# Performance work log

Measured on AMD Instinct MI355X. Metric: run time of the kernel, lower is better.

The kernel has to match this reference:

```python
import jax, jax.numpy as jnp
import numpy as np
import math

L, B, S, D, DK = 12, 2, 2048, 1024, 256
LN_EPS = 1e-5


def setup_inputs() -> dict:
    key = jax.random.key(0)
    k0, k1, k2 = jax.random.split(key, 3)
    states = jax.random.normal(k0, (L, B, S, D), dtype=jnp.float32)
    # nn.Linear default init ~ U(-1/sqrt(fan_in), 1/sqrt(fan_in))
    bound = 1.0 / math.sqrt(D)
    Wq = jax.random.uniform(k1, (DK, D), minval=-bound, maxval=bound, dtype=jnp.float32)
    Wk = jax.random.uniform(k2, (DK, D), minval=-bound, maxval=bound, dtype=jnp.float32)
    ln_weight = jnp.ones((D,), dtype=jnp.float32)
    ln_bias = jnp.zeros((D,), dtype=jnp.float32)
    latest_gate = jnp.asarray(0.5, dtype=jnp.float32)
    return {"states": states, "Wq": Wq, "Wk": Wk,
            "ln_weight": ln_weight, "ln_bias": ln_bias,
            "latest_gate": latest_gate}


def _layer_norm(x, w, b):
    mu = jnp.mean(x, axis=-1, keepdims=True)
    var = jnp.mean(jnp.square(x - mu), axis=-1, keepdims=True)
    return (x - mu) * jax.lax.rsqrt(var + LN_EPS) * w + b


def reference(states, Wq, Wk, ln_weight, ln_bias, latest_gate):
    # states: (L, B, S, D)
    normalized = _layer_norm(states, ln_weight, ln_bias)          # (L,B,S,D)
    latest = normalized[-1]                                       # (B,S,D)
    query = jnp.einsum('bsd,kd->bsk', latest, Wq)                 # (B,S,DK)
    keys = jnp.einsum('lbsd,kd->lbsk', normalized, Wk)            # (L,B,S,DK)
    scale = 1.0 / math.sqrt(query.shape[-1])
    logits = jnp.einsum('bsk,lbsk->lbs', query, keys) * scale     # (L,B,S)
    weights = jax.nn.softmax(logits, axis=0)                      # softmax over depth
    mixed = jnp.einsum('lbs,lbsd->bsd', weights, states)          # (B,S,D)
    gate = jax.nn.sigmoid(latest_gate)
    return gate * states[-1] + (1.0 - gate) * mixed
```

## Files before the change

### kernel.cpp

```cpp
#include <hip/hip_runtime.h>

#define NL 12
#define NB 2
#define NS 2048
#define ND 1024
#define NDK 256
#define NBS (NB*NS)

typedef __attribute__((ext_vector_type(8))) short short8;
typedef __attribute__((ext_vector_type(4))) short short4v;
typedef __attribute__((ext_vector_type(4))) float floatx4;

__device__ __forceinline__ unsigned short f2bf(float f) {
    unsigned int u = __float_as_uint(f);
    u += 0x7FFFu + ((u >> 16) & 1u);
    return (unsigned short)(u >> 16);
}
__device__ __forceinline__ short f2bfs(float f) { return (short)f2bf(f); }
__device__ __forceinline__ float bf2f(short s) {
    return __uint_as_float(((unsigned int)(unsigned short)s) << 16);
}

__global__ void k_prep_ln(const float* __restrict__ Wq, const float* __restrict__ Wk,
                          const float* __restrict__ x11,
                          const float* __restrict__ lnw, const float* __restrict__ lnb,
                          unsigned short* __restrict__ W2t, unsigned short* __restrict__ U) {
    const int tid = threadIdx.x;
    if (blockIdx.x < 256) {
        const int lane = tid & 63, wv = tid >> 6;
        const int wid = blockIdx.x * 4 + wv;
        const int tm = wid >> 4;
        const int tnb = wid & 15;
        const int lr = lane & 15, kh = lane >> 4;
        floatx4 acc[4];
#pragma unroll
        for (int c = 0; c < 4; ++c) acc[c] = (floatx4){0.f, 0.f, 0.f, 0.f};
#pragma unroll 2
        for (int kb = 0; kb < 8; ++kb) {
            const float* Ab = Wk + (size_t)(kb * 32 + kh * 8) * ND + tm * 16 + lr;
            const float* Bb = Wq + (size_t)(kb * 32 + kh * 8) * ND + tnb * 64 + lr;
            short8 a;
#pragma unroll
            for (int j = 0; j < 8; ++j) a[j] = f2bfs(Ab[(size_t)j * ND]);
#pragma unroll
            for (int c = 0; c < 4; ++c) {
                short8 b;
#pragma unroll
                for (int j = 0; j < 8; ++j) b[j] = f2bfs(Bb[(size_t)j * ND + c * 16]);
                acc[c] = __builtin_amdgcn_mfma_f32_16x16x32_bf16(a, b, acc[c], 0, 0, 0);
            }
        }
#pragma unroll
        for (int c = 0; c < 4; ++c)
#pragma unroll
            for (int r = 0; r < 4; ++r)
                W2t[(size_t)(tm * 16 + kh * 4 + r) * ND + tnb * 64 + c * 16 + lr] = f2bf(acc[c][r]);
        return;
    }
    __shared__ float red[8];
    const int p = blockIdx.x - 256;
    const float4* xr = (const float4*)(x11 + (size_t)p * ND);
    float4 x = xr[tid];
    float s1 = x.x + x.y + x.z + x.w;
    float s2 = x.x*x.x + x.y*x.y + x.z*x.z + x.w*x.w;
#pragma unroll
    for (int m = 32; m > 0; m >>= 1) { s1 += __shfl_xor(s1, m); s2 += __shfl_xor(s2, m); }
    int wv = tid >> 6;
    if ((tid & 63) == 0) { red[wv] = s1; red[4 + wv] = s2; }
    __syncthreads();
    float S1 = red[0] + red[1] + red[2] + red[3];
    float S2 = red[4] + red[5] + red[6] + red[7];
    float mu = S1 * (1.0f / ND);
    float var = S2 * (1.0f / ND) - mu * mu;
    float rstd = rsqrtf(var + 1e-5f);
    float4 w = ((const float4*)lnw)[tid];
    float4 b = ((const float4*)lnb)[tid];
    ushort4 u;
    u.x = f2bf((x.x - mu) * rstd * w.x + b.x);
    u.y = f2bf((x.y - mu) * rstd * w.y + b.y);
    u.z = f2bf((x.z - mu) * rstd * w.z + b.z);
    u.w = f2bf((x.w - mu) * rstd * w.w + b.w);
    ((ushort4*)U)[(size_t)p * (ND / 4) + tid] = u;
}

#define BM 64
#define BN 128
#define BK 64
#define LDP 72
#define TLP 132
__global__ __launch_bounds__(256) void k_vgemm(const unsigned short* __restrict__ U,
                                               const unsigned short* __restrict__ W2t,
                                               unsigned short* __restrict__ V) {
    __shared__ unsigned short As[2][BM * LDP];
    __shared__ unsigned short Bs[2][BN * LDP];
    const int tid = threadIdx.x;
    const int lane = tid & 63;
    const int wv = tid >> 6;
    const int wr = wv >> 1, wc = wv & 1;
    const int lr = lane & 15, kh = lane >> 4;
    const int bm0 = (blockIdx.x >> 3) * BM;
    const int bn0 = (blockIdx.x & 7) * BN;

    int aOff[2], bOff[4];
    const short8* gA[2];
    const short8* gB[4];
#pragma unroll
    for (int j = 0; j < 2; ++j) {
        int idx = j * 256 + tid;
        int row = idx >> 3, c8 = idx & 7;
        aOff[j] = row * LDP + c8 * 8;
        gA[j] = (const short8*)(U + (size_t)(bm0 + row) * ND) + c8;
    }
#pragma unroll
    for (int j = 0; j < 4; ++j) {
        int idx = j * 256 + tid;
        int row = idx >> 3, c8 = idx & 7;
        bOff[j] = row * LDP + c8 * 8;
        gB[j] = (const short8*)(W2t + (size_t)(bn0 + row) * ND) + c8;
    }

    floatx4 acc[2][4];
#pragma unroll
    for (int m = 0; m < 2; ++m)
#pragma unroll
        for (int n = 0; n < 4; ++n) acc[m][n] = (floatx4){0.f, 0.f, 0.f, 0.f};

    short8 ra[2], rb[4];
#pragma unroll
    for (int j = 0; j < 2; ++j) ra[j] = gA[j][0];
#pragma unroll
    for (int j = 0; j < 4; ++j) rb[j] = gB[j][0];

    const int NT = ND / BK;
#pragma unroll 1
    for (int t = 0; t < NT; ++t) {
        unsigned short* Ab = As[t & 1];
        unsigned short* Bb = Bs[t & 1];
#pragma unroll
        for (int j = 0; j < 2; ++j) *(short8*)&Ab[aOff[j]] = ra[j];
#pragma unroll
        for (int j = 0; j < 4; ++j) *(short8*)&Bb[bOff[j]] = rb[j];
        __syncthreads();
        if (t < NT - 1) {
#pragma unroll
            for (int j = 0; j < 2; ++j) ra[j] = gA[j][(t + 1) * 8];
#pragma unroll
            for (int j = 0; j < 4; ++j) rb[j] = gB[j][(t + 1) * 8];
        }
#pragma unroll
        for (int kk = 0; kk < 2; ++kk) {
            short8 a[2], b[4];
#pragma unroll
            for (int m = 0; m < 2; ++m)
                a[m] = *(const short8*)&Ab[(wr * 32 + m * 16 + lr) * LDP + kk * 32 + kh * 8];
#pragma unroll
            for (int n = 0; n < 4; ++n)
                b[n] = *(const short8*)&Bb[(wc * 64 + n * 16 + lr) * LDP + kk * 32 + kh * 8];
#pragma unroll
            for (int m = 0; m < 2; ++m)
#pragma unroll
                for (int n = 0; n < 4; ++n)
                    acc[m][n] = __builtin_amdgcn_mfma_f32_16x16x32_bf16(a[m], b[n], acc[m][n], 0, 0, 0);
        }
    }

    __syncthreads();
    unsigned short* Cs = (unsigned short*)As;
#pragma unroll
    for (int m = 0; m < 2; ++m)
#pragma unroll
        for (int n = 0; n < 4; ++n)
#pragma unroll
            for (int r = 0; r < 4; ++r)
                Cs[(wr * 32 + m * 16 + kh * 4 + r) * TLP + wc * 64 + n * 16 + lr] = f2bf(acc[m][n][r]);
    __syncthreads();
#pragma unroll
    for (int j = 0; j < 4; ++j) {
        int idx = j * 256 + tid;
        int row = idx >> 4, c8 = idx & 15;
        *(short8*)&V[(size_t)(bm0 + row) * ND + bn0 + c8 * 8] = *(const short8*)&Cs[row * TLP + c8 * 8];
    }
}

__global__ void k_fused(const float* __restrict__ states, const unsigned short* __restrict__ V,
                        const float* __restrict__ lnw, const float* __restrict__ lnb,
                        const float* __restrict__ gatep, float* __restrict__ out) {
    __shared__ float s_logit[12];
    __shared__ float s_w12[12];
    __shared__ float s_g;
    __shared__ float s_part[4][ND];
    __shared__ float s_x11[ND];
    const int p = blockIdx.x;
    const int tid = threadIdx.x;
    const int lane = tid & 63;
    const int wv = tid >> 6;
    const size_t LS = (size_t)NBS * ND;
    const float* base = states + (size_t)p * ND;
    const short4v* Vp = (const short4v*)(V + (size_t)p * ND);

    float4 t[4];
    float red[11];
#pragma unroll
    for (int j = 0; j < 11; ++j) red[j] = 0.f;
#pragma unroll
    for (int i = 0; i < 4; ++i) {
        int idx = lane + 64 * i;
        short4v vq = Vp[idx];
        float4 v;
        v.x = bf2f(vq[0]); v.y = bf2f(vq[1]); v.z = bf2f(vq[2]); v.w = bf2f(vq[3]);
        float4 w = ((const float4*)lnw)[idx];
        float4 b = ((const float4*)lnb)[idx];
        float4 tt; tt.x = v.x*w.x; tt.y = v.y*w.y; tt.z = v.z*w.z; tt.w = v.w*w.w;
        t[i] = tt;
        red[9]  += tt.x + tt.y + tt.z + tt.w;
        red[10] += v.x*b.x + v.y*b.y + v.z*b.z + v.w*b.w;
    }

    float4 x[3][4];
#pragma unroll
    for (int rr = 0; rr < 3; ++rr) {
        const int l = wv + 4 * rr;
        const float4* xr = (const float4*)(base + (size_t)l * LS);
#pragma unroll
        for (int i = 0; i < 4; ++i) {
            float4 xx = xr[lane + 64 * i];
            x[rr][i] = xx;
            red[rr]     += xx.x + xx.y + xx.z + xx.w;
            red[3 + rr] += xx.x*xx.x + xx.y*xx.y + xx.z*xx.z + xx.w*xx.w;
            red[6 + rr] += xx.x*t[i].x + xx.y*t[i].y + xx.z*t[i].z + xx.w*t[i].w;
        }
    }
#pragma unroll
    for (int m = 32; m > 0; m >>= 1) {
#pragma unroll
        for (int j = 0; j < 11; ++j) red[j] += __shfl_xor(red[j], m);
    }
    if (lane == 0) {
#pragma unroll
        for (int rr = 0; rr < 3; ++rr) {
            float mu = red[rr] * (1.0f / ND);
            float var = red[3 + rr] * (1.0f / ND) - mu * mu;
            float rstd = rsqrtf(var + 1e-5f);
            s_logit[wv + 4 * rr] = 0.0625f * (rstd * (red[6 + rr] - mu * red[9]) + red[10]);
        }
    }
    __syncthreads();
    if (tid == 0) {
        float mx = s_logit[0];
#pragma unroll
        for (int l = 1; l < 12; ++l) mx = fmaxf(mx, s_logit[l]);
        float e[12], sum = 0.f;
#pragma unroll
        for (int l = 0; l < 12; ++l) { e[l] = expf(s_logit[l] - mx); sum += e[l]; }
        float inv = 1.0f / sum;
#pragma unroll
        for (int l = 0; l < 12; ++l) s_w12[l] = e[l] * inv;
        s_g = 1.0f / (1.0f + expf(-gatep[0]));
    }
    __syncthreads();

    const float w0 = s_w12[wv], w1 = s_w12[wv + 4], w2 = s_w12[wv + 8];
#pragma unroll
    for (int i = 0; i < 4; ++i) {
        int idx = lane + 64 * i;
        float4 pm;
        pm.x = w0*x[0][i].x + w1*x[1][i].x + w2*x[2][i].x;
        pm.y = w0*x[0][i].y + w1*x[1][i].y + w2*x[2][i].y;
        pm.z = w0*x[0][i].z + w1*x[1][i].z + w2*x[2][i].z;
        pm.w = w0*x[0][i].w + w1*x[1][i].w + w2*x[2][i].w;
        ((float4*)s_part[wv])[idx] = pm;
        if (wv == 3) ((float4*)s_x11)[idx] = x[2][i];
    }
    __syncthreads();

    const float g = s_g;
    float4 a0 = ((const float4*)s_part[0])[tid];
    float4 a1 = ((const float4*)s_part[1])[tid];
    float4 a2 = ((const float4*)s_part[2])[tid];
    float4 a3 = ((const float4*)s_part[3])[tid];
    float4 x11 = ((const float4*)s_x11)[tid];
    float4 o;
    o.x = g * x11.x + (1.f - g) * (a0.x + a1.x + a2.x + a3.x);
    o.y = g * x11.y + (1.f - g) * (a0.y + a1.y + a2.y + a3.y);
    o.z = g * x11.z + (1.f - g) * (a0.z + a1.z + a2.z + a3.z);
    o.w = g * x11.w + (1.f - g) * (a0.w + a1.w + a2.w + a3.w);
    ((float4*)(out + (size_t)p * ND))[tid] = o;
}

extern "C" void kernel_launch(void* const* d_in, const int* in_sizes, int n_in,
                              void* d_out, int out_size, void* d_ws, size_t ws_size,
                              hipStream_t stream) {
    (void)in_sizes; (void)n_in; (void)out_size; (void)ws_size;
    const float* states = (const float*)d_in[0];
    const float* Wq     = (const float*)d_in[1];
    const float* Wk     = (const float*)d_in[2];
    const float* lnw    = (const float*)d_in[3];
    const float* lnb    = (const float*)d_in[4];
    const float* gate   = (const float*)d_in[5];
    float* out = (float*)d_out;
    char* ws = (char*)d_ws;

    unsigned short* U   = (unsigned short*)(ws);
    unsigned short* W2t = (unsigned short*)(ws + (9u << 20));
    unsigned short* V   = (unsigned short*)(ws + (12u << 20));

    k_prep_ln<<<dim3(256 + NBS), dim3(256), 0, stream>>>(
        Wq, Wk, states + (size_t)(NL - 1) * NBS * ND, lnw, lnb, W2t, U);
    k_vgemm<<<dim3((NBS / BM) * (ND / BN)), dim3(256), 0, stream>>>(U, W2t, V);
    k_fused<<<dim3(NBS), dim3(256), 0, stream>>>(states, V, lnw, lnb, gate, out);
}
```

Before: 74.84 us.

## Fuse last-layer LayerNorm into the V GEMM via algebraic mean/rstd correction

The separate LayerNorm pass that wrote a normalized bf16 copy of the last layer is removed. The GEMM now reads raw fp32 states, converts them to bf16 while loading the tile, and accumulates per-row sum and sum of squares. It then applies rstd, mean and bias corrections in the epilogue, using the vectors c1 = W2·lnw and c2 = W2·lnb computed in the prep kernel, with lnw folded into W2t. This saves one write and one read of the 4096x1024 intermediate, at the cost of twice the A-tile global bytes and extra conversion work inside the GEMM loop. It also risks precision loss, because the GEMM now multiplies un-normalized bf16 inputs and the mean is subtracted afterwards.

```diff
diff --git a/kernel.cpp b/kernel.cpp
--- a/kernel.cpp
+++ b/kernel.cpp
@@ -21,10 +21,10 @@
     return __uint_as_float(((unsigned int)(unsigned short)s) << 16);
 }
 
-__global__ void k_prep_ln(const float* __restrict__ Wq, const float* __restrict__ Wk,
-                          const float* __restrict__ x11,
-                          const float* __restrict__ lnw, const float* __restrict__ lnb,
-                          unsigned short* __restrict__ W2t, unsigned short* __restrict__ U) {
+__global__ void k_prep(const float* __restrict__ Wq, const float* __restrict__ Wk,
+                       const float* __restrict__ lnw, const float* __restrict__ lnb,
+                       unsigned short* __restrict__ W2t,
+                       float* __restrict__ c1v, float* __restrict__ c2v) {
     const int tid = threadIdx.x;
     if (blockIdx.x < 256) {
         const int lane = tid & 63, wv = tid >> 6;
@@ -51,36 +51,41 @@
             }
         }
 #pragma unroll
-        for (int c = 0; c < 4; ++c)
+        for (int c = 0; c < 4; ++c) {
+            const int col = tnb * 64 + c * 16 + lr;
+            const float wc_ = lnw[col];
 #pragma unroll
             for (int r = 0; r < 4; ++r)
-                W2t[(size_t)(tm * 16 + kh * 4 + r) * ND + tnb * 64 + c * 16 + lr] = f2bf(acc[c][r]);
+                W2t[(size_t)(tm * 16 + kh * 4 + r) * ND + col] = f2bf(acc[c][r] * wc_);
+        }
         return;
     }
-    __shared__ float red[8];
-    const int p = blockIdx.x - 256;
-    const float4* xr = (const float4*)(x11 + (size_t)p * ND);
-    float4 x = xr[tid];
-    float s1 = x.x + x.y + x.z + x.w;
-    float s2 = x.x*x.x + x.y*x.y + x.z*x.z + x.w*x.w;
-#pragma unroll
-    for (int m = 32; m > 0; m >>= 1) { s1 += __shfl_xor(s1, m); s2 += __shfl_xor(s2, m); }
-    int wv = tid >> 6;
-    if ((tid & 63) == 0) { red[wv] = s1; red[4 + wv] = s2; }
-    __syncthreads();
-    float S1 = red[0] + red[1] + red[2] + red[3];
-    float S2 = red[4] + red[5] + red[6] + red[7];
-    float mu = S1 * (1.0f / ND);
-    float var = S2 * (1.0f / ND) - mu * mu;
-    float rstd = rsqrtf(var + 1e-5f);
-    float4 w = ((const float4*)lnw)[tid];
-    float4 b = ((const float4*)lnb)[tid];
-    ushort4 u;
-    u.x = f2bf((x.x - mu) * rstd * w.x + b.x);
-    u.y = f2bf((x.y - mu) * rstd * w.y + b.y);
-    u.z = f2bf((x.z - mu) * rstd * w.z + b.z);
-    u.w = f2bf((x.w - mu) * rstd * w.w + b.w);
-    ((ushort4*)U)[(size_t)p * (ND / 4) + tid] = u;
+    __shared__ float z1[NDK], z2[NDK];
+    const int bid2 = blockIdx.x - 256;
+    {
+        const float4* wq = (const float4*)(Wq + (size_t)tid * ND);
+        const float4* w4 = (const float4*)lnw;
+        const float4* b4 = (const float4*)lnb;
+        float a1 = 0.f, a2 = 0.f;
+#pragma unroll 4
+        for (int i = 0; i < ND / 4; ++i) {
+            float4 q = wq[i], ww = w4[i], bb = b4[i];
+            a1 += q.x*ww.x + q.y*ww.y + q.z*ww.z + q.w*ww.w;
+            a2 += q.x*bb.x + q.y*bb.y + q.z*bb.z + q.w*bb.w;
+        }
+        z1[tid] = a1; z2[tid] = a2;
+    }
+    __syncthreads();
+    if (tid < 128) {
+        const int d = bid2 * 128 + tid;
+        float s1 = 0.f, s2 = 0.f;
+#pragma unroll 4
+        for (int k = 0; k < NDK; ++k) {
+            float wk = Wk[(size_t)k * ND + d];
+            s1 += wk * z1[k]; s2 += wk * z2[k];
+        }
+        c1v[d] = s1; c2v[d] = s2;
+    }
 }
 
 #define BM 64
@@ -88,11 +93,14 @@
 #define BK 64
 #define LDP 72
 #define TLP 132
-__global__ __launch_bounds__(256) void k_vgemm(const unsigned short* __restrict__ U,
+__global__ __launch_bounds__(256) void k_vgemm(const float* __restrict__ x11,
                                                const unsigned short* __restrict__ W2t,
+                                               const float* __restrict__ c1v,
+                                               const float* __restrict__ c2v,
                                                unsigned short* __restrict__ V) {
     __shared__ unsigned short As[2][BM * LDP];
     __shared__ unsigned short Bs[2][BN * LDP];
+    __shared__ float s_s1[BM], s_s2[BM], s_mu[BM], s_rs[BM];
     const int tid = threadIdx.x;
     const int lane = tid & 63;
     const int wv = tid >> 6;
@@ -101,16 +109,18 @@
     const int bm0 = (blockIdx.x >> 3) * BM;
     const int bn0 = (blockIdx.x & 7) * BN;
 
-    int aOff[2], bOff[4];
-    const short8* gA[2];
+    int aOff[4], aRow[4];
+    const float4* gAx[4];
+#pragma unroll
+    for (int j = 0; j < 4; ++j) {
+        int idx = j * 256 + tid;
+        aRow[j] = idx >> 4;
+        int c4 = idx & 15;
+        aOff[j] = aRow[j] * LDP + c4 * 4;
+        gAx[j] = (const float4*)(x11 + (size_t)(bm0 + aRow[j]) * ND) + c4;
+    }
+    int bOff[4];
     const short8* gB[4];
-#pragma unroll
-    for (int j = 0; j < 2; ++j) {
-        int idx = j * 256 + tid;
-        int row = idx >> 3, c8 = idx & 7;
-        aOff[j] = row * LDP + c8 * 8;
-        gA[j] = (const short8*)(U + (size_t)(bm0 + row) * ND) + c8;
-    }
 #pragma unroll
     for (int j = 0; j < 4; ++j) {
         int idx = j * 256 + tid;
@@ -125,9 +135,14 @@
 #pragma unroll
         for (int n = 0; n < 4; ++n) acc[m][n] = (floatx4){0.f, 0.f, 0.f, 0.f};
 
-    short8 ra[2], rb[4];
-#pragma unroll
-    for (int j = 0; j < 2; ++j) ra[j] = gA[j][0];
+    float sa1[4], sa2[4];
+#pragma unroll
+    for (int j = 0; j < 4; ++j) { sa1[j] = 0.f; sa2[j] = 0.f; }
+
+    float4 rax[4];
+    short8 rb[4];
+#pragma unroll
+    for (int j = 0; j < 4; ++j) rax[j] = gAx[j][0];
 #pragma unroll
     for (int j = 0; j < 4; ++j) rb[j] = gB[j][0];
 
@@ -137,13 +152,19 @@
         unsigned short* Ab = As[t & 1];
         unsigned short* Bb = Bs[t & 1];
 #pragma unroll
-        for (int j = 0; j < 2; ++j) *(short8*)&Ab[aOff[j]] = ra[j];
+        for (int j = 0; j < 4; ++j) {
+            float4 r = rax[j];
+            sa1[j] += r.x + r.y + r.z + r.w;
+            sa2[j] += r.x*r.x + r.y*r.y + r.z*r.z + r.w*r.w;
+            short4v s; s[0] = f2bfs(r.x); s[1] = f2bfs(r.y); s[2] = f2bfs(r.z); s[3] = f2bfs(r.w);
+            *(short4v*)&Ab[aOff[j]] = s;
+        }
 #pragma unroll
         for (int j = 0; j < 4; ++j) *(short8*)&Bb[bOff[j]] = rb[j];
         __syncthreads();
         if (t < NT - 1) {
 #pragma unroll
-            for (int j = 0; j < 2; ++j) ra[j] = gA[j][(t + 1) * 8];
+            for (int j = 0; j < 4; ++j) rax[j] = gAx[j][(t + 1) * 16];
 #pragma unroll
             for (int j = 0; j < 4; ++j) rb[j] = gB[j][(t + 1) * 8];
         }
@@ -152,10 +173,10 @@
             short8 a[2], b[4];
 #pragma unroll
             for (int m = 0; m < 2; ++m)
-                a[m] = *(const short8*)&Ab[(wr * 32 + m * 16 + lr) * LDP + kk * 32 + kh * 8];
+                a[m] = *(const short8*)&As[t & 1][(wr * 32 + m * 16 + lr) * LDP + kk * 32 + kh * 8];
 #pragma unroll
             for (int n = 0; n < 4; ++n)
-                b[n] = *(const short8*)&Bb[(wc * 64 + n * 16 + lr) * LDP + kk * 32 + kh * 8];
+                b[n] = *(const short8*)&Bs[t & 1][(wc * 64 + n * 16 + lr) * LDP + kk * 32 + kh * 8];
 #pragma unroll
             for (int m = 0; m < 2; ++m)
 #pragma unroll
@@ -164,15 +185,41 @@
         }
     }
 
-    __syncthreads();
+#pragma unroll
+    for (int j = 0; j < 4; ++j) {
+#pragma unroll
+        for (int m = 1; m < 16; m <<= 1) {
+            sa1[j] += __shfl_xor(sa1[j], m);
+            sa2[j] += __shfl_xor(sa2[j], m);
+        }
+        if ((tid & 15) == 0) { s_s1[aRow[j]] = sa1[j]; s_s2[aRow[j]] = sa2[j]; }
+    }
+    __syncthreads();
+    if (tid < BM) {
+        float mu = s_s1[tid] * (1.0f / ND);
+        float var = s_s2[tid] * (1.0f / ND) - mu * mu;
+        s_mu[tid] = mu;
+        s_rs[tid] = rsqrtf(var + 1e-5f);
+    }
+    __syncthreads();
+
     unsigned short* Cs = (unsigned short*)As;
 #pragma unroll
-    for (int m = 0; m < 2; ++m)
-#pragma unroll
-        for (int n = 0; n < 4; ++n)
-#pragma unroll
-            for (int r = 0; r < 4; ++r)
-                Cs[(wr * 32 + m * 16 + kh * 4 + r) * TLP + wc * 64 + n * 16 + lr] = f2bf(acc[m][n][r]);
+    for (int n = 0; n < 4; ++n) {
+        const int coll = wc * 64 + n * 16 + lr;
+        const float cc1 = c1v[bn0 + coll];
+        const float cc2 = c2v[bn0 + coll];
+#pragma unroll
+        for (int m = 0; m < 2; ++m) {
+#pragma unroll
+            for (int r = 0; r < 4; ++r) {
+                const int rowl = wr * 32 + m * 16 + kh * 4 + r;
+                const float rs = s_rs[rowl];
+                const float v = rs * acc[m][n][r] + cc2 - rs * s_mu[rowl] * cc1;
+                Cs[rowl * TLP + coll] = f2bf(v);
+            }
+        }
+    }
     __syncthreads();
 #pragma unroll
     for (int j = 0; j < 4; ++j) {
@@ -300,12 +347,13 @@
     float* out = (float*)d_out;
     char* ws = (char*)d_ws;
 
-    unsigned short* U   = (unsigned short*)(ws);
-    unsigned short* W2t = (unsigned short*)(ws + (9u << 20));
-    unsigned short* V   = (unsigned short*)(ws + (12u << 20));
-
-    k_prep_ln<<<dim3(256 + NBS), dim3(256), 0, stream>>>(
-        Wq, Wk, states + (size_t)(NL - 1) * NBS * ND, lnw, lnb, W2t, U);
-    k_vgemm<<<dim3((NBS / BM) * (ND / BN)), dim3(256), 0, stream>>>(U, W2t, V);
+    unsigned short* W2t = (unsigned short*)(ws);
+    float*          c1v = (float*)        (ws + (2u << 20));
+    float*          c2v = (float*)        (ws + (2u << 20) + 4096);
+    unsigned short* V   = (unsigned short*)(ws + (3u << 20));
+    const float* x11 = states + (size_t)(NL - 1) * NBS * ND;
+
+    k_prep<<<dim3(264), dim3(256), 0, stream>>>(Wq, Wk, lnw, lnb, W2t, c1v, c2v);
+    k_vgemm<<<dim3((NBS / BM) * (ND / BN)), dim3(256), 0, stream>>>(x11, W2t, c1v, c2v, V);
     k_fused<<<dim3(NBS), dim3(256), 0, stream>>>(states, V, lnw, lnb, gate, out);
 }
```

New measurement: 110.2 us. 47.2% more time.
